# Optimization experiments

Hardware: AMD Instinct MI355X
Metric: run time of the kernel (lower is better)

Reference implementation:

```python
import jax, jax.numpy as jnp
import numpy as np


def entmax15(scores, axis):
    """Exact entmax-1.5 (Peters & Martins 2019), sort-based threshold."""
    s = jnp.moveaxis(scores, axis, -1)
    s = (s - jnp.max(s, axis=-1, keepdims=True)) / 2.0
    d = s.shape[-1]
    srt = jnp.sort(s, axis=-1)[..., ::-1]  # descending
    rho = jnp.arange(1, d + 1, dtype=s.dtype)
    mean = jnp.cumsum(srt, axis=-1) / rho
    mean_sq = jnp.cumsum(srt * srt, axis=-1) / rho
    ss = rho * (mean_sq - mean * mean)
    delta = (1.0 - ss) / rho
    tau = mean - jnp.sqrt(jnp.clip(delta, 0.0, None))
    support = jnp.sum((tau <= srt).astype(jnp.int32), axis=-1)  # support size k*
    tau_star = jnp.take_along_axis(tau, (support - 1)[..., None], axis=-1)
    p = jnp.square(jnp.clip(s - tau_star, 0.0, None))
    return jnp.moveaxis(p, -1, axis)


def setup_inputs() -> dict:
    key = jax.random.key(0)
    k0, k1, k2 = jax.random.split(key, 3)
    B, S, H, A = 64, 2048, 512, 128
    lstm_output = jax.random.normal(k0, (B, S, H), dtype=jnp.float32)
    W1 = jax.random.normal(k1, (H, A), dtype=jnp.float32) * (1.0 / np.sqrt(H))
    b1 = jnp.zeros((A,), dtype=jnp.float32)
    W2 = jax.random.normal(k2, (A, 1), dtype=jnp.float32) * (1.0 / np.sqrt(A))
    b2 = jnp.zeros((1,), dtype=jnp.float32)
    return {"lstm_output": lstm_output, "W1": W1, "b1": b1, "W2": W2, "b2": b2}


def reference(lstm_output, W1, b1, W2, b2):
    # score MLP: Linear -> tanh -> Linear, squeeze(-1)
    h = jnp.tanh(lstm_output @ W1 + b1)            # [B, S, A]
    scores = (h @ W2)[..., 0] + b2[0]              # [B, S]
    weights = entmax15(scores, axis=1)             # sparse weights over seq dim
    context = jnp.einsum('bsh,bs->bh', lstm_output, weights)  # [B, H]
    return (context, weights)
```

## Files before the change

kernel.cpp:

```cpp
#include <hip/hip_runtime.h>
#include <math.h>

#define BB 64
#define SS 2048
#define HH 512
#define AA 128
#define MM (BB*SS)
#define BM 128

typedef __attribute__((ext_vector_type(8)))  short short8;
typedef __attribute__((ext_vector_type(16))) float f32x16;

__device__ inline unsigned short f2bf(float f) {
    unsigned u = __float_as_uint(f);
    unsigned r = (u + 0x7fff + ((u >> 16) & 1)) >> 16;
    return (unsigned short)r;
}
__device__ inline float bf2f(unsigned short h) {
    return __uint_as_float(((unsigned)h) << 16);
}

__global__ __launch_bounds__(256) void prep_w1t(
    const float* __restrict__ W1, unsigned short* __restrict__ W1Th,
    unsigned short* __restrict__ W1Tl)
{
    int idx = blockIdx.x * 256 + threadIdx.x;
    int n = idx & 127, k = idx >> 7;
    float v = W1[k * AA + n];
    unsigned short h = f2bf(v);
    W1Th[n * HH + k] = h;
    W1Tl[n * HH + k] = f2bf(v - bf2f(h));
}

__global__ __launch_bounds__(256) void score_mfma(
    const float* __restrict__ X,
    const unsigned short* __restrict__ W1Th,
    const unsigned short* __restrict__ W1Tl,
    const float* __restrict__ b1, const float* __restrict__ W2,
    const float* __restrict__ b2, float* __restrict__ scores)
{
    __shared__ unsigned short A_lds[2][4][BM][8];
    __shared__ unsigned short B_lds[2][4][AA][8];

    const int tid  = threadIdx.x;
    const int wave = tid >> 6;
    const int lane = tid & 63;
    const int l31  = lane & 31;
    const int half = lane >> 5;
    const int m0   = blockIdx.x * BM;

    f32x16 acc[4];
    #pragma unroll
    for (int nt = 0; nt < 4; nt++)
        #pragma unroll
        for (int j = 0; j < 16; j++) acc[nt][j] = 0.f;

    for (int k0 = 0; k0 < HH; k0 += 32) {
        const int kq = tid & 7;
        const int g  = kq >> 1;
        const int jo = (kq & 1) * 4;
        #pragma unroll
        for (int i = 0; i < 4; i++) {
            int m = (tid >> 3) + 32 * i;
            float4 f = *(const float4*)(X + (size_t)(m0 + m) * HH + k0 + kq * 4);
            unsigned short h0 = f2bf(f.x), h1 = f2bf(f.y),
                           h2 = f2bf(f.z), h3 = f2bf(f.w);
            ushort4 hv = {h0, h1, h2, h3};
            ushort4 lv = {f2bf(f.x - bf2f(h0)), f2bf(f.y - bf2f(h1)),
                          f2bf(f.z - bf2f(h2)), f2bf(f.w - bf2f(h3))};
            int msw = m ^ (g << 1);
            *(ushort4*)&A_lds[0][g][msw][jo] = hv;
            *(ushort4*)&A_lds[1][g][msw][jo] = lv;
        }
        #pragma unroll
        for (int i = 0; i < 4; i++) {
            int c    = tid + 256 * i;
            int hilo = c >> 9;
            int gg   = (c >> 7) & 3;
            int n    = c & 127;
            const unsigned short* src = hilo ? W1Tl : W1Th;
            short8 v = *(const short8*)(src + (size_t)n * HH + k0 + gg * 8);
            *(short8*)&B_lds[hilo][gg][n][0] = v;
        }
        __syncthreads();

        #pragma unroll
        for (int s = 0; s < 2; s++) {
            int gr  = s * 2 + half;
            int mr  = wave * 32 + l31;
            short8 a_h = *(const short8*)&A_lds[0][gr][mr ^ (gr << 1)][0];
            short8 a_l = *(const short8*)&A_lds[1][gr][mr ^ (gr << 1)][0];
            #pragma unroll
            for (int nt = 0; nt < 4; nt++) {
                int nr = nt * 32 + l31;
                short8 b_h = *(const short8*)&B_lds[0][gr][nr][0];
                short8 b_l = *(const short8*)&B_lds[1][gr][nr][0];
                acc[nt] = __builtin_amdgcn_mfma_f32_32x32x16_bf16(a_h, b_h, acc[nt], 0, 0, 0);
                acc[nt] = __builtin_amdgcn_mfma_f32_32x32x16_bf16(a_h, b_l, acc[nt], 0, 0, 0);
                acc[nt] = __builtin_amdgcn_mfma_f32_32x32x16_bf16(a_l, b_h, acc[nt], 0, 0, 0);
            }
        }
        __syncthreads();
    }

    float part[16];
    #pragma unroll
    for (int r = 0; r < 16; r++) part[r] = 0.f;
    #pragma unroll
    for (int nt = 0; nt < 4; nt++) {
        int n = nt * 32 + l31;
        float bias = b1[n];
        float w2   = W2[n];
        #pragma unroll
        for (int r = 0; r < 16; r++)
            part[r] += tanhf(acc[nt][r] + bias) * w2;
    }
    #pragma unroll
    for (int off = 16; off > 0; off >>= 1)
        #pragma unroll
        for (int r = 0; r < 16; r++)
            part[r] += __shfl_xor(part[r], off);
    if (l31 == 0) {
        float bb2 = b2[0];
        #pragma unroll
        for (int r = 0; r < 16; r++) {
            int row = (r & 3) + 8 * (r >> 2) + 4 * half;
            scores[m0 + wave * 32 + row] = part[r] + bb2;
        }
    }
}

__global__ __launch_bounds__(1024) void entmax_kernel(
    const float* __restrict__ scores, float* __restrict__ weights)
{
    __shared__ float s_orig[SS];
    __shared__ float srt[SS];
    __shared__ float tau[SS];
    __shared__ float sp[1024];
    __shared__ float sq[1024];
    __shared__ float red[16];
    __shared__ int   s_cnt;
    __shared__ float s_max, s_taustar;

    const int t = threadIdx.x;
    const int b = blockIdx.x;
    const float* row = scores + (size_t)b * SS;

    float v0 = row[t];
    float v1 = row[t + 1024];

    float mx = fmaxf(v0, v1);
    #pragma unroll
    for (int off = 32; off > 0; off >>= 1)
        mx = fmaxf(mx, __shfl_down(mx, off, 64));
    if ((t & 63) == 0) red[t >> 6] = mx;
    __syncthreads();
    if (t < 16) {
        float m = red[t];
        #pragma unroll
        for (int off = 8; off > 0; off >>= 1)
            m = fmaxf(m, __shfl_down(m, off, 16));
        if (t == 0) s_max = m;
    }
    __syncthreads();
    mx = s_max;
    v0 = (v0 - mx) * 0.5f;
    v1 = (v1 - mx) * 0.5f;
    s_orig[t]        = v0;
    s_orig[t + 1024] = v1;
    srt[t]           = v0;
    srt[t + 1024]    = v1;
    __syncthreads();

    for (int k = 2; k <= SS; k <<= 1) {
        for (int j = k >> 1; j > 0; j >>= 1) {
            #pragma unroll
            for (int u = 0; u < 2; u++) {
                int i = t + 1024 * u;
                int p = i ^ j;
                if (p > i) {
                    float a = srt[i], c = srt[p];
                    bool up = ((i & k) == 0);
                    if (up ? (a < c) : (a > c)) { srt[i] = c; srt[p] = a; }
                }
            }
            __syncthreads();
        }
    }

    float e0 = srt[2 * t], e1 = srt[2 * t + 1];
    sp[t] = e0 + e1;
    sq[t] = e0 * e0 + e1 * e1;
    __syncthreads();
    for (int off = 1; off < 1024; off <<= 1) {
        float ap = 0.f, aq = 0.f;
        if (t >= off) { ap = sp[t - off]; aq = sq[t - off]; }
        __syncthreads();
        sp[t] += ap; sq[t] += aq;
        __syncthreads();
    }
    float excl_p = (t > 0) ? sp[t - 1] : 0.f;
    float excl_q = (t > 0) ? sq[t - 1] : 0.f;

    int cnt_local = 0;
    float tau0, tau1;
    {
        float c0  = excl_p + e0;
        float c0q = excl_q + e0 * e0;
        float rho = (float)(2 * t + 1);
        float mean   = c0 / rho;
        float meansq = c0q / rho;
        float ssv    = rho * (meansq - mean * mean);
        float delta  = (1.f - ssv) / rho;
        tau0 = mean - sqrtf(fmaxf(delta, 0.f));
        cnt_local += (tau0 <= e0) ? 1 : 0;

        float c1  = c0 + e1;
        float c1q = c0q + e1 * e1;
        rho = (float)(2 * t + 2);
        mean   = c1 / rho;
        meansq = c1q / rho;
        ssv    = rho * (meansq - mean * mean);
        delta  = (1.f - ssv) / rho;
        tau1 = mean - sqrtf(fmaxf(delta, 0.f));
        cnt_local += (tau1 <= e1) ? 1 : 0;
    }
    tau[2 * t]     = tau0;
    tau[2 * t + 1] = tau1;
    if (t == 0) s_cnt = 0;
    __syncthreads();

    int c = cnt_local;
    #pragma unroll
    for (int off = 32; off > 0; off >>= 1) c += __shfl_down(c, off, 64);
    if ((t & 63) == 0) atomicAdd(&s_cnt, c);
    __syncthreads();
    if (t == 0) s_taustar = tau[s_cnt - 1];
    __syncthreads();
    float ts = s_taustar;

    float w0 = fmaxf(s_orig[t] - ts, 0.f);
    float w1 = fmaxf(s_orig[t + 1024] - ts, 0.f);
    weights[(size_t)b * SS + t]        = w0 * w0;
    weights[(size_t)b * SS + t + 1024] = w1 * w1;
}

__global__ __launch_bounds__(256) void context_kernel(
    const float* __restrict__ X, const float* __restrict__ weights,
    float* __restrict__ ctx)
{
    const int b = blockIdx.y;
    const int chunk = blockIdx.x;
    const int tid = threadIdx.x;
    const float* wrow  = weights + (size_t)b * SS + chunk * 64;
    const float* xbase = X + ((size_t)b * SS + (size_t)chunk * 64) * HH;
    float acc0 = 0.f, acc1 = 0.f;
    bool any = false;
    for (int s = 0; s < 64; s++) {
        float w = wrow[s];
        if (w != 0.f) {
            any = true;
            float2 x = *(const float2*)(xbase + (size_t)s * HH + 2 * tid);
            acc0 = fmaf(x.x, w, acc0);
            acc1 = fmaf(x.y, w, acc1);
        }
    }
    if (any) {
        atomicAdd(&ctx[b * HH + 2 * tid],     acc0);
        atomicAdd(&ctx[b * HH + 2 * tid + 1], acc1);
    }
}

extern "C" void kernel_launch(void* const* d_in, const int* in_sizes, int n_in,
                              void* d_out, int out_size, void* d_ws, size_t ws_size,
                              hipStream_t stream) {
    const float* X  = (const float*)d_in[0];
    const float* W1 = (const float*)d_in[1];
    const float* b1 = (const float*)d_in[2];
    const float* W2 = (const float*)d_in[3];
    const float* b2 = (const float*)d_in[4];

    float* out     = (float*)d_out;
    float* ctx     = out;
    float* weights = out + BB * HH;
    float* scores  = weights;

    unsigned short* W1Th = (unsigned short*)d_ws;
    unsigned short* W1Tl = W1Th + (size_t)AA * HH;

    hipMemsetAsync(ctx, 0, (size_t)BB * HH * sizeof(float), stream);
    prep_w1t<<<dim3(256), 256, 0, stream>>>(W1, W1Th, W1Tl);
    score_mfma<<<dim3(MM / BM), 256, 0, stream>>>(X, W1Th, W1Tl, b1, W2, b2, scores);
    entmax_kernel<<<dim3(BB), 1024, 0, stream>>>(scores, weights);
    context_kernel<<<dim3(32, BB), 256, 0, stream>>>(X, weights, ctx);
}
```

Baseline: 424.4 us.

## Rewrite score GEMM with register-direct A, double-buffered B, and bisection entmax

The score GEMM now loads X straight from global memory into MFMA operand registers and splits it into bf16 hi/lo there, so A no longer goes through LDS. It doubles the block tile to 256 rows, double-buffers the W1 tiles in LDS with prefetch, and uses a fast exp-based tanh. The sort-based entmax kernel (bitonic sort plus scan) is replaced by a 32-step bisection search for tau over register-resident values. This removes LDS traffic and many barriers, but bisection gives an approximate threshold, the lo residual is truncated rather than rounded, and fast_tanh is less accurate.

After: 403.2 us. -5.0%, faster.

```diff
diff --git a/kernel.cpp b/kernel.cpp
--- a/kernel.cpp
+++ b/kernel.cpp
@@ -6,12 +6,11 @@
 #define HH 512
 #define AA 128
 #define MM (BB*SS)
-#define BM 128
 
 typedef __attribute__((ext_vector_type(8)))  short short8;
 typedef __attribute__((ext_vector_type(16))) float f32x16;
 
-__device__ inline unsigned short f2bf(float f) {
+__device__ inline unsigned short f2bf_rne(float f) {
     unsigned u = __float_as_uint(f);
     unsigned r = (u + 0x7fff + ((u >> 16) & 1)) >> 16;
     return (unsigned short)r;
@@ -19,6 +18,10 @@
 __device__ inline float bf2f(unsigned short h) {
     return __uint_as_float(((unsigned)h) << 16);
 }
+__device__ inline float fast_tanh(float x) {
+    float t = __expf(2.0f * x);
+    return 1.0f - 2.0f * __builtin_amdgcn_rcpf(t + 1.0f);
+}
 
 __global__ __launch_bounds__(256) void prep_w1t(
     const float* __restrict__ W1, unsigned short* __restrict__ W1Th,
@@ -27,222 +30,208 @@
     int idx = blockIdx.x * 256 + threadIdx.x;
     int n = idx & 127, k = idx >> 7;
     float v = W1[k * AA + n];
-    unsigned short h = f2bf(v);
+    unsigned short h = f2bf_rne(v);
     W1Th[n * HH + k] = h;
-    W1Tl[n * HH + k] = f2bf(v - bf2f(h));
-}
-
-__global__ __launch_bounds__(256) void score_mfma(
+    W1Tl[n * HH + k] = f2bf_rne(v - bf2f(h));
+}
+
+__global__ __launch_bounds__(256, 2) void score_mfma(
     const float* __restrict__ X,
     const unsigned short* __restrict__ W1Th,
     const unsigned short* __restrict__ W1Tl,
     const float* __restrict__ b1, const float* __restrict__ W2,
     const float* __restrict__ b2, float* __restrict__ scores)
 {
-    __shared__ unsigned short A_lds[2][4][BM][8];
-    __shared__ unsigned short B_lds[2][4][AA][8];
+    __shared__ unsigned short B_lds[2][2][4][AA][8];
 
     const int tid  = threadIdx.x;
     const int wave = tid >> 6;
     const int lane = tid & 63;
     const int l31  = lane & 31;
     const int half = lane >> 5;
-    const int m0   = blockIdx.x * BM;
-
-    f32x16 acc[4];
-    #pragma unroll
-    for (int nt = 0; nt < 4; nt++)
-        #pragma unroll
-        for (int j = 0; j < 16; j++) acc[nt][j] = 0.f;
-
-    for (int k0 = 0; k0 < HH; k0 += 32) {
-        const int kq = tid & 7;
-        const int g  = kq >> 1;
-        const int jo = (kq & 1) * 4;
-        #pragma unroll
-        for (int i = 0; i < 4; i++) {
-            int m = (tid >> 3) + 32 * i;
-            float4 f = *(const float4*)(X + (size_t)(m0 + m) * HH + k0 + kq * 4);
-            unsigned short h0 = f2bf(f.x), h1 = f2bf(f.y),
-                           h2 = f2bf(f.z), h3 = f2bf(f.w);
-            ushort4 hv = {h0, h1, h2, h3};
-            ushort4 lv = {f2bf(f.x - bf2f(h0)), f2bf(f.y - bf2f(h1)),
-                          f2bf(f.z - bf2f(h2)), f2bf(f.w - bf2f(h3))};
-            int msw = m ^ (g << 1);
-            *(ushort4*)&A_lds[0][g][msw][jo] = hv;
-            *(ushort4*)&A_lds[1][g][msw][jo] = lv;
-        }
-        #pragma unroll
-        for (int i = 0; i < 4; i++) {
-            int c    = tid + 256 * i;
-            int hilo = c >> 9;
-            int gg   = (c >> 7) & 3;
-            int n    = c & 127;
-            const unsigned short* src = hilo ? W1Tl : W1Th;
-            short8 v = *(const short8*)(src + (size_t)n * HH + k0 + gg * 8);
-            *(short8*)&B_lds[hilo][gg][n][0] = v;
+    const int m0   = blockIdx.x * 256;
+
+    int sb_hilo[4], sb_g[4], sb_n[4];
+    #pragma unroll
+    for (int i = 0; i < 4; i++) {
+        int c = tid + 256 * i;
+        sb_hilo[i] = c >> 9;
+        sb_g[i]    = (c >> 7) & 3;
+        sb_n[i]    = c & 127;
+    }
+
+    const float* aptr0 = X + (size_t)(m0 + wave * 64      + l31) * HH + half * 8;
+    const float* aptr1 = X + (size_t)(m0 + wave * 64 + 32 + l31) * HH + half * 8;
+
+    f32x16 acc[2][4];
+    #pragma unroll
+    for (int mt = 0; mt < 2; mt++)
+        #pragma unroll
+        for (int nt = 0; nt < 4; nt++)
+            #pragma unroll
+            for (int j = 0; j < 16; j++) acc[mt][nt][j] = 0.f;
+
+    short8 breg[4];
+    float4 apre[2][2][2];
+
+    #pragma unroll
+    for (int i = 0; i < 4; i++) {
+        const unsigned short* src = sb_hilo[i] ? W1Tl : W1Th;
+        breg[i] = *(const short8*)(src + (size_t)sb_n[i] * HH + sb_g[i] * 8);
+    }
+    #pragma unroll
+    for (int s = 0; s < 2; s++) {
+        apre[0][s][0] = *(const float4*)(aptr0 + s * 16);
+        apre[0][s][1] = *(const float4*)(aptr0 + s * 16 + 4);
+        apre[1][s][0] = *(const float4*)(aptr1 + s * 16);
+        apre[1][s][1] = *(const float4*)(aptr1 + s * 16 + 4);
+    }
+    #pragma unroll
+    for (int i = 0; i < 4; i++)
+        *(short8*)&B_lds[0][sb_hilo[i]][sb_g[i]][sb_n[i]][0] = breg[i];
+    __syncthreads();
+
+    for (int it = 0; it < 16; it++) {
+        const int cur = it & 1;
+
+        if (it < 15) {
+            #pragma unroll
+            for (int i = 0; i < 4; i++) {
+                const unsigned short* src = sb_hilo[i] ? W1Tl : W1Th;
+                breg[i] = *(const short8*)(src + (size_t)sb_n[i] * HH
+                                           + (it + 1) * 32 + sb_g[i] * 8);
+            }
+        }
+
+        short8 ah[2][2], al[2][2];
+        #pragma unroll
+        for (int mt = 0; mt < 2; mt++)
+            #pragma unroll
+            for (int s = 0; s < 2; s++) {
+                float fs[8];
+                *(float4*)&fs[0] = apre[mt][s][0];
+                *(float4*)&fs[4] = apre[mt][s][1];
+                #pragma unroll
+                for (int j = 0; j < 8; j++) {
+                    unsigned short h = f2bf_rne(fs[j]);
+                    ah[mt][s][j] = (short)h;
+                    float r = fs[j] - bf2f(h);
+                    al[mt][s][j] = (short)(__float_as_uint(r) >> 16);
+                }
+            }
+
+        if (it < 15) {
+            #pragma unroll
+            for (int s = 0; s < 2; s++) {
+                apre[0][s][0] = *(const float4*)(aptr0 + (it + 1) * 32 + s * 16);
+                apre[0][s][1] = *(const float4*)(aptr0 + (it + 1) * 32 + s * 16 + 4);
+                apre[1][s][0] = *(const float4*)(aptr1 + (it + 1) * 32 + s * 16);
+                apre[1][s][1] = *(const float4*)(aptr1 + (it + 1) * 32 + s * 16 + 4);
+            }
+        }
+
+        #pragma unroll
+        for (int s = 0; s < 2; s++) {
+            const int gr = s * 2 + half;
+            #pragma unroll
+            for (int nt = 0; nt < 4; nt++) {
+                short8 bh = *(const short8*)&B_lds[cur][0][gr][nt * 32 + l31][0];
+                short8 bl = *(const short8*)&B_lds[cur][1][gr][nt * 32 + l31][0];
+                acc[0][nt] = __builtin_amdgcn_mfma_f32_32x32x16_bf16(ah[0][s], bh, acc[0][nt], 0, 0, 0);
+                acc[0][nt] = __builtin_amdgcn_mfma_f32_32x32x16_bf16(ah[0][s], bl, acc[0][nt], 0, 0, 0);
+                acc[0][nt] = __builtin_amdgcn_mfma_f32_32x32x16_bf16(al[0][s], bh, acc[0][nt], 0, 0, 0);
+                acc[1][nt] = __builtin_amdgcn_mfma_f32_32x32x16_bf16(ah[1][s], bh, acc[1][nt], 0, 0, 0);
+                acc[1][nt] = __builtin_amdgcn_mfma_f32_32x32x16_bf16(ah[1][s], bl, acc[1][nt], 0, 0, 0);
+                acc[1][nt] = __builtin_amdgcn_mfma_f32_32x32x16_bf16(al[1][s], bh, acc[1][nt], 0, 0, 0);
+            }
+        }
+
+        if (it < 15) {
+            #pragma unroll
+            for (int i = 0; i < 4; i++)
+                *(short8*)&B_lds[cur ^ 1][sb_hilo[i]][sb_g[i]][sb_n[i]][0] = breg[i];
         }
         __syncthreads();
-
-        #pragma unroll
-        for (int s = 0; s < 2; s++) {
-            int gr  = s * 2 + half;
-            int mr  = wave * 32 + l31;
-            short8 a_h = *(const short8*)&A_lds[0][gr][mr ^ (gr << 1)][0];
-            short8 a_l = *(const short8*)&A_lds[1][gr][mr ^ (gr << 1)][0];
-            #pragma unroll
-            for (int nt = 0; nt < 4; nt++) {
-                int nr = nt * 32 + l31;
-                short8 b_h = *(const short8*)&B_lds[0][gr][nr][0];
-                short8 b_l = *(const short8*)&B_lds[1][gr][nr][0];
-                acc[nt] = __builtin_amdgcn_mfma_f32_32x32x16_bf16(a_h, b_h, acc[nt], 0, 0, 0);
-                acc[nt] = __builtin_amdgcn_mfma_f32_32x32x16_bf16(a_h, b_l, acc[nt], 0, 0, 0);
-                acc[nt] = __builtin_amdgcn_mfma_f32_32x32x16_bf16(a_l, b_h, acc[nt], 0, 0, 0);
-            }
-        }
+    }
+
+    const float bb2 = b2[0];
+    #pragma unroll
+    for (int mt = 0; mt < 2; mt++) {
+        float part[16];
+        #pragma unroll
+        for (int r = 0; r < 16; r++) part[r] = 0.f;
+        #pragma unroll
+        for (int nt = 0; nt < 4; nt++) {
+            int n = nt * 32 + l31;
+            float bias = b1[n];
+            float w2   = W2[n];
+            #pragma unroll
+            for (int r = 0; r < 16; r++)
+                part[r] += fast_tanh(acc[mt][nt][r] + bias) * w2;
+        }
+        #pragma unroll
+        for (int off = 16; off > 0; off >>= 1)
+            #pragma unroll
+            for (int r = 0; r < 16; r++)
+                part[r] += __shfl_xor(part[r], off);
+        if (l31 == 0) {
+            #pragma unroll
+            for (int r = 0; r < 16; r++) {
+                int row = (r & 3) + 8 * (r >> 2) + 4 * half;
+                scores[m0 + wave * 64 + mt * 32 + row] = part[r] + bb2;
+            }
+        }
+    }
+}
+
+__global__ __launch_bounds__(256) void entmax_bisect(
+    const float* __restrict__ scores, float* __restrict__ weights)
+{
+    __shared__ float red[4];
+    const int t = threadIdx.x, b = blockIdx.x;
+    const int wv = t >> 6, ln = t & 63;
+    const float* row = scores + (size_t)b * SS;
+
+    float v[8];
+    #pragma unroll
+    for (int i = 0; i < 8; i++) v[i] = row[t + 256 * i];
+
+    float mx = v[0];
+    #pragma unroll
+    for (int i = 1; i < 8; i++) mx = fmaxf(mx, v[i]);
+    #pragma unroll
+    for (int off = 32; off > 0; off >>= 1) mx = fmaxf(mx, __shfl_xor(mx, off));
+    if (ln == 0) red[wv] = mx;
+    __syncthreads();
+    mx = fmaxf(fmaxf(red[0], red[1]), fmaxf(red[2], red[3]));
+
+    #pragma unroll
+    for (int i = 0; i < 8; i++) v[i] = (v[i] - mx) * 0.5f;
+
+    float lo = -1.0f, hi = 0.0f;
+    for (int it = 0; it < 32; it++) {
+        float tm = 0.5f * (lo + hi);
+        float s = 0.f;
+        #pragma unroll
+        for (int i = 0; i < 8; i++) {
+            float d = fmaxf(v[i] - tm, 0.f);
+            s = fmaf(d, d, s);
+        }
+        #pragma unroll
+        for (int off = 32; off > 0; off >>= 1) s += __shfl_xor(s, off);
         __syncthreads();
-    }
-
-    float part[16];
-    #pragma unroll
-    for (int r = 0; r < 16; r++) part[r] = 0.f;
-    #pragma unroll
-    for (int nt = 0; nt < 4; nt++) {
-        int n = nt * 32 + l31;
-        float bias = b1[n];
-        float w2   = W2[n];
-        #pragma unroll
-        for (int r = 0; r < 16; r++)
-            part[r] += tanhf(acc[nt][r] + bias) * w2;
-    }
-    #pragma unroll
-    for (int off = 16; off > 0; off >>= 1)
-        #pragma unroll
-        for (int r = 0; r < 16; r++)
-            part[r] += __shfl_xor(part[r], off);
-    if (l31 == 0) {
-        float bb2 = b2[0];
-        #pragma unroll
-        for (int r = 0; r < 16; r++) {
-            int row = (r & 3) + 8 * (r >> 2) + 4 * half;
-            scores[m0 + wave * 32 + row] = part[r] + bb2;
-        }
-    }
-}
-
-__global__ __launch_bounds__(1024) void entmax_kernel(
-    const float* __restrict__ scores, float* __restrict__ weights)
-{
-    __shared__ float s_orig[SS];
-    __shared__ float srt[SS];
-    __shared__ float tau[SS];
-    __shared__ float sp[1024];
-    __shared__ float sq[1024];
-    __shared__ float red[16];
-    __shared__ int   s_cnt;
-    __shared__ float s_max, s_taustar;
-
-    const int t = threadIdx.x;
-    const int b = blockIdx.x;
-    const float* row = scores + (size_t)b * SS;
-
-    float v0 = row[t];
-    float v1 = row[t + 1024];
-
-    float mx = fmaxf(v0, v1);
-    #pragma unroll
-    for (int off = 32; off > 0; off >>= 1)
-        mx = fmaxf(mx, __shfl_down(mx, off, 64));
-    if ((t & 63) == 0) red[t >> 6] = mx;
-    __syncthreads();
-    if (t < 16) {
-        float m = red[t];
-        #pragma unroll
-        for (int off = 8; off > 0; off >>= 1)
-            m = fmaxf(m, __shfl_down(m, off, 16));
-        if (t == 0) s_max = m;
-    }
-    __syncthreads();
-    mx = s_max;
-    v0 = (v0 - mx) * 0.5f;
-    v1 = (v1 - mx) * 0.5f;
-    s_orig[t]        = v0;
-    s_orig[t + 1024] = v1;
-    srt[t]           = v0;
-    srt[t + 1024]    = v1;
-    __syncthreads();
-
-    for (int k = 2; k <= SS; k <<= 1) {
-        for (int j = k >> 1; j > 0; j >>= 1) {
-            #pragma unroll
-            for (int u = 0; u < 2; u++) {
-                int i = t + 1024 * u;
-                int p = i ^ j;
-                if (p > i) {
-                    float a = srt[i], c = srt[p];
-                    bool up = ((i & k) == 0);
-                    if (up ? (a < c) : (a > c)) { srt[i] = c; srt[p] = a; }
-                }
-            }
-            __syncthreads();
-        }
-    }
-
-    float e0 = srt[2 * t], e1 = srt[2 * t + 1];
-    sp[t] = e0 + e1;
-    sq[t] = e0 * e0 + e1 * e1;
-    __syncthreads();
-    for (int off = 1; off < 1024; off <<= 1) {
-        float ap = 0.f, aq = 0.f;
-        if (t >= off) { ap = sp[t - off]; aq = sq[t - off]; }
+        if (ln == 0) red[wv] = s;
         __syncthreads();
-        sp[t] += ap; sq[t] += aq;
-        __syncthreads();
-    }
-    float excl_p = (t > 0) ? sp[t - 1] : 0.f;
-    float excl_q = (t > 0) ? sq[t - 1] : 0.f;
-
-    int cnt_local = 0;
-    float tau0, tau1;
-    {
-        float c0  = excl_p + e0;
-        float c0q = excl_q + e0 * e0;
-        float rho = (float)(2 * t + 1);
-        float mean   = c0 / rho;
-        float meansq = c0q / rho;
-        float ssv    = rho * (meansq - mean * mean);
-        float delta  = (1.f - ssv) / rho;
-        tau0 = mean - sqrtf(fmaxf(delta, 0.f));
-        cnt_local += (tau0 <= e0) ? 1 : 0;
-
-        float c1  = c0 + e1;
-        float c1q = c0q + e1 * e1;
-        rho = (float)(2 * t + 2);
-        mean   = c1 / rho;
-        meansq = c1q / rho;
-        ssv    = rho * (meansq - mean * mean);
-        delta  = (1.f - ssv) / rho;
-        tau1 = mean - sqrtf(fmaxf(delta, 0.f));
-        cnt_local += (tau1 <= e1) ? 1 : 0;
-    }
-    tau[2 * t]     = tau0;
-    tau[2 * t + 1] = tau1;
-    if (t == 0) s_cnt = 0;
-    __syncthreads();
-
-    int c = cnt_local;
-    #pragma unroll
-    for (int off = 32; off > 0; off >>= 1) c += __shfl_down(c, off, 64);
-    if ((t & 63) == 0) atomicAdd(&s_cnt, c);
-    __syncthreads();
-    if (t == 0) s_taustar = tau[s_cnt - 1];
-    __syncthreads();
-    float ts = s_taustar;
-
-    float w0 = fmaxf(s_orig[t] - ts, 0.f);
-    float w1 = fmaxf(s_orig[t + 1024] - ts, 0.f);
-    weights[(size_t)b * SS + t]        = w0 * w0;
-    weights[(size_t)b * SS + t + 1024] = w1 * w1;
+        s = red[0] + red[1] + red[2] + red[3];
+        if (s >= 1.0f) lo = tm; else hi = tm;
+    }
+    float tau = 0.5f * (lo + hi);
+
+    #pragma unroll
+    for (int i = 0; i < 8; i++) {
+        float d = fmaxf(v[i] - tau, 0.f);
+        weights[(size_t)b * SS + t + 256 * i] = d * d;
+    }
 }
 
 __global__ __launch_bounds__(256) void context_kernel(
@@ -290,7 +279,7 @@
 
     hipMemsetAsync(ctx, 0, (size_t)BB * HH * sizeof(float), stream);
     prep_w1t<<<dim3(256), 256, 0, stream>>>(W1, W1Th, W1Tl);
-    score_mfma<<<dim3(MM / BM), 256, 0, stream>>>(X, W1Th, W1Tl, b1, W2, b2, scores);
-    entmax_kernel<<<dim3(BB), 1024, 0, stream>>>(scores, weights);
+    score_mfma<<<dim3(MM / 256), 256, 0, stream>>>(X, W1Th, W1Tl, b1, W2, b2, scores);
+    entmax_bisect<<<dim3(BB), 256, 0, stream>>>(scores, weights);
     context_kernel<<<dim3(32, BB), 256, 0, stream>>>(X, weights, ctx);
 }
```
